# Kernel optimization log

Measured on AMD Instinct MI355X. Metric: run time of the kernel, lower is better.

Reference implementation:

```python
import jax, jax.numpy as jnp
import numpy as np

N, E, G, L, D = 50000, 800000, 512, 3, 128
BN_EPS = 1e-5


def setup_inputs() -> dict:
    key = jax.random.key(0)
    ks = jax.random.split(key, 16)
    x = jax.random.normal(ks[0], (N, D), dtype=jnp.float32)
    edge_index = jax.random.randint(ks[1], (2, E), 0, N)
    batch = jnp.sort(jax.random.randint(ks[2], (N,), 0, G))
    W1 = jax.random.normal(ks[3], (L, D, D), dtype=jnp.float32) * 0.05
    b1 = jax.random.normal(ks[4], (L, D), dtype=jnp.float32) * 0.05
    gamma = jax.random.uniform(ks[5], (L, D), dtype=jnp.float32) + 0.5
    beta = jax.random.normal(ks[6], (L, D), dtype=jnp.float32) * 0.05
    running_mean = jax.random.normal(ks[7], (L, D), dtype=jnp.float32) * 0.1
    running_var = jax.random.uniform(ks[8], (L, D), dtype=jnp.float32) + 0.5
    W2 = jax.random.normal(ks[9], (L, D, D), dtype=jnp.float32) * 0.05
    b2 = jax.random.normal(ks[10], (L, D), dtype=jnp.float32) * 0.05
    lin1_W = jax.random.normal(ks[11], (L * D, L * D), dtype=jnp.float32) * 0.05
    lin1_b = jax.random.normal(ks[12], (L * D,), dtype=jnp.float32) * 0.05
    lin2_W = jax.random.normal(ks[13], (L * D, 10), dtype=jnp.float32) * 0.05
    lin2_b = jax.random.normal(ks[14], (10,), dtype=jnp.float32) * 0.05
    return {"x": x, "edge_index": edge_index, "batch": batch,
            "W1": W1, "b1": b1, "gamma": gamma, "beta": beta,
            "running_mean": running_mean, "running_var": running_var,
            "W2": W2, "b2": b2, "lin1_W": lin1_W, "lin1_b": lin1_b,
            "lin2_W": lin2_W, "lin2_b": lin2_b}


def _gin_layer(h, src, dst, W1, b1, gamma, beta, rm, rv, W2, b2):
    # GINConv (eps=0): MLP((1+eps)*x + sum_{j->i} x_j); aggregate src->dst
    agg = jax.ops.segment_sum(h[src], dst, num_segments=N)  # [N, D]
    z = (h + agg) @ W1 + b1
    # BatchNorm1d in eval mode (running stats)
    z = (z - rm) * (gamma / jnp.sqrt(rv + BN_EPS)) + beta
    z = jax.nn.relu(z)
    return jax.nn.relu(z @ W2 + b2)


def reference(x, edge_index, batch, W1, b1, gamma, beta, running_mean,
              running_var, W2, b2, lin1_W, lin1_b, lin2_W, lin2_b):
    src, dst = edge_index[0], edge_index[1]
    h = x
    pooled = []
    for i in range(L):
        h = _gin_layer(h, src, dst, W1[i], b1[i], gamma[i], beta[i],
                       running_mean[i], running_var[i], W2[i], b2[i])
        pooled.append(jax.ops.segment_sum(h, batch, num_segments=G))  # [G, D]
    g = jnp.concatenate(pooled, axis=1)  # [G, L*D]
    g = jax.nn.relu(g @ lin1_W + lin1_b)
    # dropout is identity in eval mode
    return g @ lin2_W + lin2_b  # [G, num_classes]
```

## Files before the change

### kernel.cpp

```cpp
#include <hip/hip_runtime.h>
#include <hip/hip_bf16.h>

#define D_FEAT 128
#define N_GRAPHS 512
#define N_LAYERS 3
#define POOL_DIM (N_LAYERS * D_FEAT)
#define N_CLASSES 10
#define BN_EPS 1e-5f
#define CAP 64
#define NBINS 8
#define SLABCAP 768


typedef __attribute__((ext_vector_type(8))) short bf16x8;
typedef __attribute__((ext_vector_type(8))) unsigned short ushort8;
typedef __attribute__((ext_vector_type(4))) float f32x4;

__device__ __forceinline__ unsigned short f2bf(float f) {
    unsigned u = __builtin_bit_cast(unsigned, f);
    u += 0x7FFFu + ((u >> 16) & 1u);
    return (unsigned short)(u >> 16);
}
__device__ __forceinline__ float bf2f(unsigned short h) {
    unsigned u = ((unsigned)h) << 16;
    return __builtin_bit_cast(float, u);
}
__device__ __forceinline__ float bf_lo(unsigned u) {
    return __builtin_bit_cast(float, u << 16);
}
__device__ __forceinline__ float bf_hi(unsigned u) {
    return __builtin_bit_cast(float, u & 0xffff0000u);
}

__global__ __launch_bounds__(256) void setup_kernel(
        const float* __restrict__ x, unsigned short* __restrict__ xb,
        const float* __restrict__ W1, const float* __restrict__ W2,
        unsigned short* __restrict__ Wt,
        const float* __restrict__ b1, const float* __restrict__ gamma,
        const float* __restrict__ beta, const float* __restrict__ rm,
        const float* __restrict__ rv, const float* __restrict__ b2,
        float* __restrict__ ea, float* __restrict__ eb,
        int* __restrict__ cursor, float* __restrict__ pooled,
        const int* __restrict__ ei, int2* __restrict__ pairs,
        int* __restrict__ cnts, int E,
        int N, int n4, int B0, int B1, int B2, int B3, int B4) {
    int b = blockIdx.x, tid = threadIdx.x;
    if (b < B0) {
        int i = b * 256 + tid;
        if (i < n4) {
            float4 v = ((const float4*)x)[i];
            ushort4 o;
            o.x = f2bf(v.x); o.y = f2bf(v.y); o.z = f2bf(v.z); o.w = f2bf(v.w);
            ((ushort4*)xb)[i] = o;
        }
    } else if (b < B1) {
        int idx = (b - B0) * 256 + tid;
        int slot = idx >> 14;
        int r = (idx >> 7) & 127;
        int c = idx & 127;
        int l = slot >> 1;
        const float* W = (slot & 1) ? W2 : W1;
        Wt[idx] = f2bf(W[(size_t)l * D_FEAT * D_FEAT + (size_t)c * D_FEAT + r]);
    } else if (b < B2) {
        int i = (b - B1) * 256 + tid;
        if (i < N_LAYERS * D_FEAT) {
            int l = i >> 7, c = i & 127;
            float s = gamma[i] * rsqrtf(rv[i] + BN_EPS);
            ea[(2 * l) * D_FEAT + c] = s;
            eb[(2 * l) * D_FEAT + c] = (b1[i] - rm[i]) * s + beta[i];
            ea[(2 * l + 1) * D_FEAT + c] = 1.0f;
            eb[(2 * l + 1) * D_FEAT + c] = b2[i];
        }
    } else if (b < B3) {
        int i = (b - B2) * 256 + tid;
        if (i < N) cursor[i] = 0;
    } else if (b < B4) {
        int i = (b - B3) * 256 + tid;
        if (i < N_GRAPHS * POOL_DIM) pooled[i] = 0.f;
    } else {
        __shared__ int loc[NBINS];
        int bb = b - B4;
        int per = (E + 255) / 256;
        int e0 = bb * per;
        int e1 = e0 + per; if (e1 > E) e1 = E;
        int span = (N + NBINS - 1) / NBINS;
        if (tid < NBINS) loc[tid] = 0;
        __syncthreads();
        for (int e = e0 + tid; e < e1; e += 256) {
            int dst = ei[E + e];
            int src = ei[e];
            int bin = dst / span;
            int p = atomicAdd(&loc[bin], 1);
            if (p < SLABCAP)
                pairs[((size_t)(bin * 256 + bb)) * SLABCAP + p] = make_int2(src, dst);
        }
        __syncthreads();
        if (tid < NBINS)
            cnts[tid * 256 + bb] = loc[tid];
    }
}

__global__ __launch_bounds__(256) void fill_v3(const int2* __restrict__ pairs,
                                               const int* __restrict__ cnts,
                                               int* __restrict__ cursor,
                                               int* __restrict__ bucket) {
    int r = blockIdx.x & 7;
    int chunk = blockIdx.x >> 3;
    #pragma unroll
    for (int s = 0; s < 4; ++s) {
        int blk = chunk * 4 + s;
        int cnt = cnts[r * 256 + blk];
        if (cnt > SLABCAP) cnt = SLABCAP;
        const int2* slab = pairs + (size_t)(r * 256 + blk) * SLABCAP;
        for (int p = threadIdx.x; p < cnt; p += 256) {
            int2 pr = slab[p];
            int pos = atomicAdd(&cursor[pr.y], 1);
            if (pos < CAP) bucket[(size_t)pr.y * CAP + pos] = pr.x;
        }
    }
}

__global__ __launch_bounds__(256) void agg_kernel(const unsigned short* __restrict__ hprev,
                                                  const int* __restrict__ deg,
                                                  const int* __restrict__ bucket,
                                                  unsigned short* __restrict__ y, int n) {
    int wave = threadIdx.x >> 6, lane = threadIdx.x & 63;
    int n0 = (blockIdx.x * 4 + wave) * 2;
    if (n0 >= n) return;
    int n1 = n0 + 1;
    bool v1 = (n1 < n);
    int d0 = deg[n0]; if (d0 > CAP) d0 = CAP;
    int d1 = v1 ? deg[n1] : 0; if (d1 > CAP) d1 = CAP;
    int grp = lane >> 4, sub = lane & 15;
    const uint4* hp = (const uint4*)hprev;

    int idx0 = bucket[(size_t)n0 * CAP + lane];
    int idx1 = v1 ? bucket[(size_t)n1 * CAP + lane] : 0;

    uint4 s0v = hp[(size_t)n0 * 16 + sub];
    uint4 s1v = v1 ? hp[(size_t)n1 * 16 + sub] : make_uint4(0u, 0u, 0u, 0u);

    float a0[8] = {0.f,0.f,0.f,0.f,0.f,0.f,0.f,0.f};
    float a1[8] = {0.f,0.f,0.f,0.f,0.f,0.f,0.f,0.f};
    int dmax = d0 > d1 ? d0 : d1;

    auto issue = [&](int t, bool (&p0)[4], bool (&p1)[4],
                     uint4 (&w0)[4], uint4 (&w1)[4]) {
        #pragma unroll
        for (int q = 0; q < 4; ++q) {
            int e = t + q * 4 + grp;
            int s0 = __shfl(idx0, e & 63);
            int s1 = __shfl(idx1, e & 63);
            p0[q] = e < d0;
            p1[q] = e < d1;
            int r0 = p0[q] ? s0 : n0;
            int r1 = p1[q] ? s1 : n0;
            w0[q] = hp[(size_t)r0 * 16 + sub];
            w1[q] = hp[(size_t)r1 * 16 + sub];
        }
    };
    auto accum = [&](bool (&p0)[4], bool (&p1)[4],
                     uint4 (&w0)[4], uint4 (&w1)[4]) {
        #pragma unroll
        for (int q = 0; q < 4; ++q) {
            if (p0[q]) {
                uint4 v = w0[q];
                a0[0] += bf_lo(v.x); a0[1] += bf_hi(v.x);
                a0[2] += bf_lo(v.y); a0[3] += bf_hi(v.y);
                a0[4] += bf_lo(v.z); a0[5] += bf_hi(v.z);
                a0[6] += bf_lo(v.w); a0[7] += bf_hi(v.w);
            }
            if (p1[q]) {
                uint4 v = w1[q];
                a1[0] += bf_lo(v.x); a1[1] += bf_hi(v.x);
                a1[2] += bf_lo(v.y); a1[3] += bf_hi(v.y);
                a1[4] += bf_lo(v.z); a1[5] += bf_hi(v.z);
                a1[6] += bf_lo(v.w); a1[7] += bf_hi(v.w);
            }
        }
    };

    if (dmax > 0) {
        bool cp0[4], cp1[4];
        uint4 cw0[4], cw1[4];
        issue(0, cp0, cp1, cw0, cw1);
        for (int t = 16; t < dmax; t += 16) {
            bool np0[4], np1[4];
            uint4 nw0[4], nw1[4];
            issue(t, np0, np1, nw0, nw1);
            accum(cp0, cp1, cw0, cw1);
            #pragma unroll
            for (int q = 0; q < 4; ++q) {
                cp0[q] = np0[q]; cp1[q] = np1[q];
                cw0[q] = nw0[q]; cw1[q] = nw1[q];
            }
        }
        accum(cp0, cp1, cw0, cw1);
    }

    #pragma unroll
    for (int j = 0; j < 8; ++j) {
        a0[j] += __shfl_xor(a0[j], 16);
        a0[j] += __shfl_xor(a0[j], 32);
        a1[j] += __shfl_xor(a1[j], 16);
        a1[j] += __shfl_xor(a1[j], 32);
    }

    a0[0] += bf_lo(s0v.x); a0[1] += bf_hi(s0v.x);
    a0[2] += bf_lo(s0v.y); a0[3] += bf_hi(s0v.y);
    a0[4] += bf_lo(s0v.z); a0[5] += bf_hi(s0v.z);
    a0[6] += bf_lo(s0v.w); a0[7] += bf_hi(s0v.w);
    if (v1) {
        a1[0] += bf_lo(s1v.x); a1[1] += bf_hi(s1v.x);
        a1[2] += bf_lo(s1v.y); a1[3] += bf_hi(s1v.y);
        a1[4] += bf_lo(s1v.z); a1[5] += bf_hi(s1v.z);
        a1[6] += bf_lo(s1v.w); a1[7] += bf_hi(s1v.w);
    }

    if (grp == 0) {
        uint4 o;
        o.x = (unsigned)f2bf(a0[0]) | ((unsigned)f2bf(a0[1]) << 16);
        o.y = (unsigned)f2bf(a0[2]) | ((unsigned)f2bf(a0[3]) << 16);
        o.z = (unsigned)f2bf(a0[4]) | ((unsigned)f2bf(a0[5]) << 16);
        o.w = (unsigned)f2bf(a0[6]) | ((unsigned)f2bf(a0[7]) << 16);
        ((uint4*)y)[(size_t)n0 * 16 + sub] = o;
        if (v1) {
            uint4 p;
            p.x = (unsigned)f2bf(a1[0]) | ((unsigned)f2bf(a1[1]) << 16);
            p.y = (unsigned)f2bf(a1[2]) | ((unsigned)f2bf(a1[3]) << 16);
            p.z = (unsigned)f2bf(a1[4]) | ((unsigned)f2bf(a1[5]) << 16);
            p.w = (unsigned)f2bf(a1[6]) | ((unsigned)f2bf(a1[7]) << 16);
            ((uint4*)y)[(size_t)n1 * 16 + sub] = p;
        }
    }
}

__global__ __launch_bounds__(256) void layer_fused(const unsigned short* __restrict__ A,
                                                   const unsigned short* __restrict__ Wt1,
                                                   const unsigned short* __restrict__ Wt2,
                                                   const float* __restrict__ ea1,
                                                   const float* __restrict__ eb1,
                                                   const float* __restrict__ ea2,
                                                   const float* __restrict__ eb2,
                                                   const int* __restrict__ batch,
                                                   float* __restrict__ pooled, int loff,
                                                   unsigned short* __restrict__ outh, int n) {
    __shared__ unsigned short As[64][136];
    __shared__ unsigned short Ws[128][136];
    __shared__ int bgsh[64];
    int tid = threadIdx.x;
    int row0 = blockIdx.x * 64;
    int wave = tid >> 6, lane = tid & 63;
    int m0 = wave * 16;
    int lrow = lane & 15, lq = lane >> 4;

    #pragma unroll
    for (int i = 0; i < 4; ++i) {
        int idx = tid + i * 256;
        int r = idx >> 4, c = (idx & 15) * 8;
        ushort8 v = (ushort8)0;
        if (row0 + r < n) v = *(const ushort8*)&A[(size_t)(row0 + r) * D_FEAT + c];
        *(ushort8*)&As[r][c] = v;
    }
    #pragma unroll
    for (int i = 0; i < 8; ++i) {
        int idx = tid + i * 256;
        int r = idx >> 4, c = (idx & 15) * 8;
        *(ushort8*)&Ws[r][c] = *(const ushort8*)&Wt1[(size_t)r * D_FEAT + c];
    }
    if (tid < 64)
        bgsh[tid] = (row0 + tid < n) ? batch[row0 + tid] : -1;

    ushort8 w2reg[8];
    #pragma unroll
    for (int i = 0; i < 8; ++i) {
        int idx = tid + i * 256;
        int r = idx >> 4, c = (idx & 15) * 8;
        w2reg[i] = *(const ushort8*)&Wt2[(size_t)r * D_FEAT + c];
    }
    __syncthreads();

    f32x4 acc[8] = {};
    #pragma unroll
    for (int t = 0; t < 4; ++t) {
        bf16x8 a = *(const bf16x8*)&As[m0 + lrow][t * 32 + lq * 8];
        #pragma unroll
        for (int nt = 0; nt < 8; ++nt) {
            bf16x8 b = *(const bf16x8*)&Ws[nt * 16 + lrow][t * 32 + lq * 8];
            acc[nt] = __builtin_amdgcn_mfma_f32_16x16x32_bf16(a, b, acc[nt], 0, 0, 0);
        }
    }
    __syncthreads();

    #pragma unroll
    for (int nt = 0; nt < 8; ++nt) {
        int col = nt * 16 + lrow;
        float al = ea1[col], be = eb1[col];
        #pragma unroll
        for (int r = 0; r < 4; ++r) {
            float v = fmaxf(fmaf(acc[nt][r], al, be), 0.f);
            As[m0 + lq * 4 + r][col] = f2bf(v);
        }
    }
    #pragma unroll
    for (int i = 0; i < 8; ++i) {
        int idx = tid + i * 256;
        int r = idx >> 4, c = (idx & 15) * 8;
        *(ushort8*)&Ws[r][c] = w2reg[i];
    }
    __syncthreads();

    f32x4 acc2[8] = {};
    #pragma unroll
    for (int t = 0; t < 4; ++t) {
        bf16x8 a = *(const bf16x8*)&As[m0 + lrow][t * 32 + lq * 8];
        #pragma unroll
        for (int nt = 0; nt < 8; ++nt) {
            bf16x8 b = *(const bf16x8*)&Ws[nt * 16 + lrow][t * 32 + lq * 8];
            acc2[nt] = __builtin_amdgcn_mfma_f32_16x16x32_bf16(a, b, acc2[nt], 0, 0, 0);
        }
    }

    #pragma unroll
    for (int nt = 0; nt < 8; ++nt) {
        int col = nt * 16 + lrow;
        float al = ea2[col], be = eb2[col];
        #pragma unroll
        for (int r = 0; r < 4; ++r) {
            int grow = row0 + m0 + lq * 4 + r;
            if (grow < n) {
                float v = fmaxf(fmaf(acc2[nt][r], al, be), 0.f);
                outh[(size_t)grow * D_FEAT + col] = f2bf(v);
            }
        }
    }

    __syncthreads();
    float* Wsf = (float*)Ws;
    #pragma unroll
    for (int nt = 0; nt < 8; ++nt) {
        int col = nt * 16 + lrow;
        float al = ea2[col], be = eb2[col];
        #pragma unroll
        for (int r = 0; r < 4; ++r) {
            int lr = m0 + lq * 4 + r;
            float v = fmaxf(fmaf(acc2[nt][r], al, be), 0.f);
            Wsf[lr * 132 + col] = bf2f(f2bf(v));
        }
    }
    __syncthreads();

    int c = tid & 127, half = tid >> 7;
    int rbeg = half * 32, rend = rbeg + 32;
    int cur = -1; float sum = 0.f;
    for (int r = rbeg; r < rend; ++r) {
        int g = bgsh[r];
        if (g != cur) {
            if (cur >= 0) atomicAdd(&pooled[(size_t)cur * POOL_DIM + loff + c], sum);
            cur = g; sum = 0.f;
        }
        if (g >= 0) sum += Wsf[r * 132 + c];
    }
    if (cur >= 0) atomicAdd(&pooled[(size_t)cur * POOL_DIM + loff + c], sum);
}

__global__ __launch_bounds__(256) void head_kernel(const float* __restrict__ pooled,
                                                   const float* __restrict__ W1,
                                                   const float* __restrict__ b1v,
                                                   const float* __restrict__ W2,
                                                   const float* __restrict__ b2v,
                                                   float* __restrict__ out) {
    __shared__ float pr[POOL_DIM];
    __shared__ float f1[POOL_DIM];
    __shared__ float red[256];
    int g = blockIdx.x, tid = threadIdx.x;
    for (int i = tid; i < POOL_DIM; i += 256)
        pr[i] = pooled[(size_t)g * POOL_DIM + i];
    __syncthreads();
    for (int j = tid; j < POOL_DIM; j += 256) {
        float s = b1v[j];
        for (int k = 0; k < POOL_DIM; ++k)
            s = fmaf(pr[k], W1[(size_t)k * POOL_DIM + j], s);
        f1[j] = fmaxf(s, 0.f);
    }
    __syncthreads();
    float part = 0.f;
    int c = tid / 25;
    int r = tid % 25;
    if (tid < 250) {
        for (int k = r; k < POOL_DIM; k += 25)
            part = fmaf(f1[k], W2[(size_t)k * N_CLASSES + c], part);
    }
    red[tid] = part;
    __syncthreads();
    if (tid < N_CLASSES) {
        float s = b2v[tid];
        #pragma unroll
        for (int i = 0; i < 25; ++i) s += red[tid * 25 + i];
        out[(size_t)g * N_CLASSES + tid] = s;
    }
}

extern "C" void kernel_launch(void* const* d_in, const int* in_sizes, int n_in,
                              void* d_out, int out_size, void* d_ws, size_t ws_size,
                              hipStream_t stream) {
    const float* x      = (const float*)d_in[0];
    const int*   ei     = (const int*)  d_in[1];
    const int*   batch  = (const int*)  d_in[2];
    const float* W1     = (const float*)d_in[3];
    const float* b1     = (const float*)d_in[4];
    const float* gamma  = (const float*)d_in[5];
    const float* beta   = (const float*)d_in[6];
    const float* rm     = (const float*)d_in[7];
    const float* rv     = (const float*)d_in[8];
    const float* W2     = (const float*)d_in[9];
    const float* b2     = (const float*)d_in[10];
    const float* lin1W  = (const float*)d_in[11];
    const float* lin1b  = (const float*)d_in[12];
    const float* lin2W  = (const float*)d_in[13];
    const float* lin2b  = (const float*)d_in[14];
    float* out = (float*)d_out;

    const int N = in_sizes[0] / D_FEAT;
    const int E = in_sizes[1] / 2;

    char* ws = (char*)d_ws;
    auto carve = [&](size_t bytes) {
        char* p = ws;
        ws += (bytes + 255) & ~(size_t)255;
        return p;
    };
    int*   cursor    = (int*)  carve((size_t)N * 4);
    int*   cnts      = (int*)  carve((size_t)NBINS * 256 * 4);
    int*   bucket    = (int*)  carve((size_t)N * CAP * 4);
    int2*  pairs     = (int2*) carve((size_t)NBINS * 256 * SLABCAP * 8);
    float* ea        = (float*)carve((size_t)2 * N_LAYERS * D_FEAT * 4);
    float* eb        = (float*)carve((size_t)2 * N_LAYERS * D_FEAT * 4);
    unsigned short* Wt   = (unsigned short*)carve((size_t)2 * N_LAYERS * D_FEAT * D_FEAT * 2);
    unsigned short* xb   = (unsigned short*)carve((size_t)N * D_FEAT * 2);
    unsigned short* ybuf = (unsigned short*)carve((size_t)N * D_FEAT * 2);
    unsigned short* hbuf = (unsigned short*)carve((size_t)N * D_FEAT * 2);
    float* pooled    = (float*)carve((size_t)N_GRAPHS * POOL_DIM * 4);

    const int n4 = N * D_FEAT / 4;
    const int B0 = (n4 + 255) / 256;
    const int B1 = B0 + (2 * N_LAYERS * D_FEAT * D_FEAT) / 256;
    const int B2 = B1 + 2;
    const int B3 = B2 + (N + 255) / 256;
    const int B4 = B3 + (N_GRAPHS * POOL_DIM + 255) / 256;
    const int B5 = B4 + 256;

    setup_kernel<<<B5, 256, 0, stream>>>(x, xb, W1, W2, Wt, b1, gamma, beta,
                                         rm, rv, b2, ea, eb, cursor, pooled,
                                         ei, pairs, cnts, E,
                                         N, n4, B0, B1, B2, B3, B4);
    fill_v3<<<8 * 64, 256, 0, stream>>>(pairs, cnts, cursor, bucket);

    const unsigned short* hprev = xb;
    for (int l = 0; l < N_LAYERS; ++l) {
        agg_kernel<<<(N + 7) / 8, 256, 0, stream>>>(hprev, cursor, bucket, ybuf, N);
        layer_fused<<<(N + 63) / 64, 256, 0, stream>>>(ybuf,
                      Wt + (size_t)(2 * l) * D_FEAT * D_FEAT,
                      Wt + (size_t)(2 * l + 1) * D_FEAT * D_FEAT,
                      ea + (size_t)(2 * l) * D_FEAT,
                      eb + (size_t)(2 * l) * D_FEAT,
                      ea + (size_t)(2 * l + 1) * D_FEAT,
                      eb + (size_t)(2 * l + 1) * D_FEAT,
                      batch, pooled, l * D_FEAT, hbuf, N);
        hprev = hbuf;
    }
    head_kernel<<<N_GRAPHS, 256, 0, stream>>>(pooled, lin1W, lin1b, lin2W, lin2b, out);
}
```

Before: 350.0 us.

## Batch graphs in head kernel, tile weight transpose, skip final layer output

The head kernel now handles 8 graphs per block, so each lin1 weight load feeds 8 accumulators instead of one and the weight traffic drops. The weight transpose-and-convert setup now uses 64x64 shared-memory tiles, giving coalesced reads where it previously did strided global reads. The last GIN layer no longer writes its node features to global memory, since only the pooled sums are used afterwards. The trade-offs are fewer head blocks (64) with more registers per thread, and a larger shared-memory footprint in setup_kernel.

```diff
diff --git a/kernel.cpp b/kernel.cpp
--- a/kernel.cpp
+++ b/kernel.cpp
@@ -10,6 +10,7 @@
 #define CAP 64
 #define NBINS 8
 #define SLABCAP 768
+#define GPB 8
 
 
 typedef __attribute__((ext_vector_type(8))) short bf16x8;
@@ -54,13 +55,24 @@
             ((ushort4*)xb)[i] = o;
         }
     } else if (b < B1) {
-        int idx = (b - B0) * 256 + tid;
-        int slot = idx >> 14;
-        int r = (idx >> 7) & 127;
-        int c = idx & 127;
+        __shared__ float tile[64][65];
+        int t = b - B0;
+        int slot = t >> 2;
+        int r0 = ((t >> 1) & 1) * 64;
+        int c0 = (t & 1) * 64;
         int l = slot >> 1;
         const float* W = (slot & 1) ? W2 : W1;
-        Wt[idx] = f2bf(W[(size_t)l * D_FEAT * D_FEAT + (size_t)c * D_FEAT + r]);
+        const float* Wb = W + (size_t)l * D_FEAT * D_FEAT;
+        int rr = tid >> 2, cc4 = (tid & 3) * 16;
+        #pragma unroll
+        for (int j = 0; j < 16; ++j)
+            tile[rr][cc4 + j] = Wb[(size_t)(r0 + rr) * D_FEAT + c0 + cc4 + j];
+        __syncthreads();
+        int nn = tid >> 2, kk4 = (tid & 3) * 16;
+        unsigned short* Wo = Wt + (size_t)slot * D_FEAT * D_FEAT;
+        #pragma unroll
+        for (int j = 0; j < 16; ++j)
+            Wo[(size_t)(c0 + nn) * D_FEAT + r0 + kk4 + j] = f2bf(tile[kk4 + j][nn]);
     } else if (b < B2) {
         int i = (b - B1) * 256 + tid;
         if (i < N_LAYERS * D_FEAT) {
@@ -321,16 +333,18 @@
         }
     }
 
-    #pragma unroll
-    for (int nt = 0; nt < 8; ++nt) {
-        int col = nt * 16 + lrow;
-        float al = ea2[col], be = eb2[col];
-        #pragma unroll
-        for (int r = 0; r < 4; ++r) {
-            int grow = row0 + m0 + lq * 4 + r;
-            if (grow < n) {
-                float v = fmaxf(fmaf(acc2[nt][r], al, be), 0.f);
-                outh[(size_t)grow * D_FEAT + col] = f2bf(v);
+    if (outh) {
+        #pragma unroll
+        for (int nt = 0; nt < 8; ++nt) {
+            int col = nt * 16 + lrow;
+            float al = ea2[col], be = eb2[col];
+            #pragma unroll
+            for (int r = 0; r < 4; ++r) {
+                int grow = row0 + m0 + lq * 4 + r;
+                if (grow < n) {
+                    float v = fmaxf(fmaf(acc2[nt][r], al, be), 0.f);
+                    outh[(size_t)grow * D_FEAT + col] = f2bf(v);
+                }
             }
         }
     }
@@ -370,34 +384,31 @@
                                                    const float* __restrict__ W2,
                                                    const float* __restrict__ b2v,
                                                    float* __restrict__ out) {
-    __shared__ float pr[POOL_DIM];
-    __shared__ float f1[POOL_DIM];
-    __shared__ float red[256];
-    int g = blockIdx.x, tid = threadIdx.x;
-    for (int i = tid; i < POOL_DIM; i += 256)
-        pr[i] = pooled[(size_t)g * POOL_DIM + i];
+    __shared__ float pr[GPB][POOL_DIM];
+    __shared__ float f1[GPB][POOL_DIM];
+    int g0 = blockIdx.x * GPB, tid = threadIdx.x;
+    for (int i = tid; i < GPB * POOL_DIM; i += 256)
+        pr[i / POOL_DIM][i % POOL_DIM] = pooled[(size_t)g0 * POOL_DIM + i];
     __syncthreads();
     for (int j = tid; j < POOL_DIM; j += 256) {
-        float s = b1v[j];
+        float s[GPB];
+        #pragma unroll
+        for (int g = 0; g < GPB; ++g) s[g] = b1v[j];
+        for (int k = 0; k < POOL_DIM; ++k) {
+            float w = W1[(size_t)k * POOL_DIM + j];
+            #pragma unroll
+            for (int g = 0; g < GPB; ++g) s[g] = fmaf(pr[g][k], w, s[g]);
+        }
+        #pragma unroll
+        for (int g = 0; g < GPB; ++g) f1[g][j] = fmaxf(s[g], 0.f);
+    }
+    __syncthreads();
+    if (tid < GPB * N_CLASSES) {
+        int g = tid / N_CLASSES, c = tid % N_CLASSES;
+        float s = b2v[c];
         for (int k = 0; k < POOL_DIM; ++k)
-            s = fmaf(pr[k], W1[(size_t)k * POOL_DIM + j], s);
-        f1[j] = fmaxf(s, 0.f);
-    }
-    __syncthreads();
-    float part = 0.f;
-    int c = tid / 25;
-    int r = tid % 25;
-    if (tid < 250) {
-        for (int k = r; k < POOL_DIM; k += 25)
-            part = fmaf(f1[k], W2[(size_t)k * N_CLASSES + c], part);
-    }
-    red[tid] = part;
-    __syncthreads();
-    if (tid < N_CLASSES) {
-        float s = b2v[tid];
-        #pragma unroll
-        for (int i = 0; i < 25; ++i) s += red[tid * 25 + i];
-        out[(size_t)g * N_CLASSES + tid] = s;
+            s = fmaf(f1[g][k], W2[(size_t)k * N_CLASSES + c], s);
+        out[(size_t)(g0 + g) * N_CLASSES + c] = s;
     }
 }
 
@@ -444,7 +455,7 @@
 
     const int n4 = N * D_FEAT / 4;
     const int B0 = (n4 + 255) / 256;
-    const int B1 = B0 + (2 * N_LAYERS * D_FEAT * D_FEAT) / 256;
+    const int B1 = B0 + 24;
     const int B2 = B1 + 2;
     const int B3 = B2 + (N + 255) / 256;
     const int B4 = B3 + (N_GRAPHS * POOL_DIM + 255) / 256;
@@ -459,6 +470,7 @@
     const unsigned short* hprev = xb;
     for (int l = 0; l < N_LAYERS; ++l) {
         agg_kernel<<<(N + 7) / 8, 256, 0, stream>>>(hprev, cursor, bucket, ybuf, N);
+        unsigned short* outh = (l == N_LAYERS - 1) ? nullptr : hbuf;
         layer_fused<<<(N + 63) / 64, 256, 0, stream>>>(ybuf,
                       Wt + (size_t)(2 * l) * D_FEAT * D_FEAT,
                       Wt + (size_t)(2 * l + 1) * D_FEAT * D_FEAT,
@@ -466,8 +478,8 @@
                       eb + (size_t)(2 * l) * D_FEAT,
                       ea + (size_t)(2 * l + 1) * D_FEAT,
                       eb + (size_t)(2 * l + 1) * D_FEAT,
-                      batch, pooled, l * D_FEAT, hbuf, N);
+                      batch, pooled, l * D_FEAT, outh, N);
         hprev = hbuf;
     }
-    head_kernel<<<N_GRAPHS, 256, 0, stream>>>(pooled, lin1W, lin1b, lin2W, lin2b, out);
-}
+    head_kernel<<<N_GRAPHS / GPB, 256, 0, stream>>>(pooled, lin1W, lin1b, lin2W, lin2b, out);
+}
```

Measured after the change: 370.5 us. 5.9% more time.
